# Optimization experiments

Measured on AMD Instinct MI355X. Metric: run time of the kernel, lower is better.

The kernel has to match this reference:

```python
import jax, jax.numpy as jnp
import numpy as np

T, N, H = 256, 64, 512
DT, GAMMA, EPS = 0.01, 1.0, 1.0

def setup_inputs() -> dict:
    key = jax.random.key(0)
    ks = jax.random.split(key, 6)
    s = 1.0 / np.sqrt(H)  # keep recurrent dynamics stable
    return {
        "x": jax.random.normal(ks[0], (T, N, H), jnp.float32),
        "connection_matrix": (jax.random.uniform(ks[1], (N, N)) < 0.5).astype(jnp.float32),
        "W_h": jax.random.normal(ks[2], (N, H, H), jnp.float32) * s,
        "W_x": jax.random.normal(ks[3], (N, H, H), jnp.float32) * s,
        "b": jax.random.normal(ks[4], (N, H), jnp.float32) * 0.1,
        "initial_states": jnp.zeros((N, 2, H), jnp.float32),
    }

def reference(x, connection_matrix, W_h, W_x, b, initial_states):
    # x: (T, N, H); states: (N, 2, H) with states[:,0] = h_y (the archetype output)
    def step(carry, x_t):
        states, outs = carry
        # message passing: mix previous outputs through the connection matrix,
        # then gate with the external input (elementwise)
        new_ins = (connection_matrix @ outs) * x_t                      # (N, H)
        hy, hz = states[:, 0], states[:, 1]
        # batched RON cell over all N archetypes
        pre = (jnp.einsum('nij,nj->ni', W_h, hy)
               + jnp.einsum('nij,nj->ni', W_x, new_ins) + b)            # (N, H)
        hz_n = hz + DT * (jnp.tanh(pre) - GAMMA * hy - EPS * hz)
        hy_n = hy + DT * hz_n
        new_states = jnp.stack([hy_n, hz_n], axis=1)                    # (N, 2, H)
        return (new_states, hy_n), (new_states, new_ins)

    init_outs = jnp.zeros_like(x[0])  # initial_outs=None path in the original
    _, (states_seq, ins_seq) = jax.lax.scan(step, (initial_states, init_outs), x)
    # original prepends the initial state and x[0] to the returned lists
    states_all = jnp.concatenate([initial_states[None], states_seq], axis=0)  # (T+1, N, 2, H)
    ins_all = jnp.concatenate([x[:1], ins_seq], axis=0)                       # (T+1, N, H)
    return states_all, ins_all
```

## Files before the change

### kernel.cpp

```cpp
#include <hip/hip_runtime.h>

constexpr int   T_ = 256, N_ = 64, H_ = 512;
constexpr float DT_ = 0.01f, GAMMA_ = 1.0f, EPS_ = 1.0f;

constexpr int GRID  = 256;
constexpr int BLOCK = 1024;
constexpr int WGPN  = GRID / N_;
constexpr int ROWS  = H_ / WGPN;
constexpr int WAVES = BLOCK / 64;
constexpr int RPW   = ROWS / WAVES;
constexpr int LJ    = 4;

__device__ __forceinline__ void grid_barrier(unsigned* cnt, unsigned* gen,
                                             unsigned target) {
    __syncthreads();
    if (threadIdx.x == 0) {
        __threadfence();
        unsigned prev = __hip_atomic_fetch_add(cnt, 1u, __ATOMIC_ACQ_REL,
                                               __HIP_MEMORY_SCOPE_AGENT);
        if (prev == (unsigned)GRID - 1u) {
            __hip_atomic_store(cnt, 0u, __ATOMIC_RELAXED,
                               __HIP_MEMORY_SCOPE_AGENT);
            __hip_atomic_fetch_add(gen, 1u, __ATOMIC_RELEASE,
                                   __HIP_MEMORY_SCOPE_AGENT);
        } else {
            while (__hip_atomic_load(gen, __ATOMIC_ACQUIRE,
                                     __HIP_MEMORY_SCOPE_AGENT) < target)
                __builtin_amdgcn_s_sleep(1);
        }
    }
    __syncthreads();
    __threadfence();
}

__global__ __launch_bounds__(BLOCK, 4)
void archetypes_persistent(const float* __restrict__ x,
                           const float* __restrict__ conn,
                           const float* __restrict__ W_h,
                           const float* __restrict__ W_x,
                           const float* __restrict__ bias,
                           const float* __restrict__ init_states,
                           float* __restrict__ out,
                           unsigned* __restrict__ bar)
{
    const int tid  = threadIdx.x;
    const int wg   = blockIdx.x;
    const int n    = wg / WGPN;
    const int q    = wg % WGPN;
    const int lane = tid & 63;
    const int wave = tid >> 6;

    float* states_all = out;
    float* ins_all    = out + (size_t)(T_ + 1) * N_ * 2 * H_;

    __shared__ float s_wx[LJ * WAVES][H_];
    __shared__ float s_hy[H_];
    __shared__ float s_ins[H_];
    __shared__ float s_pre[ROWS];
    __shared__ float s_conn[N_];
    __shared__ float s_bias[ROWS];

    const float4* Wh4 = (const float4*)(W_h + ((size_t)n * H_ + q * ROWS) * H_);
    const float4* Wx4 = (const float4*)(W_x + ((size_t)n * H_ + q * ROWS) * H_);

    float4 wh_reg[RPW][2];
    float4 wx_reg[RPW - LJ][2];
    #pragma unroll
    for (int j = 0; j < RPW; ++j) {
        const int r_l = wave + WAVES * j;
        wh_reg[j][0] = Wh4[r_l * (H_ / 4) + lane];
        wh_reg[j][1] = Wh4[r_l * (H_ / 4) + 64 + lane];
    }
    #pragma unroll
    for (int j = LJ; j < RPW; ++j) {
        const int r_l = wave + WAVES * j;
        wx_reg[j - LJ][0] = Wx4[r_l * (H_ / 4) + lane];
        wx_reg[j - LJ][1] = Wx4[r_l * (H_ / 4) + 64 + lane];
    }
    {
        float4* dst = (float4*)&s_wx[0][0];
        for (int idx = tid; idx < LJ * WAVES * (H_ / 4); idx += BLOCK)
            dst[idx] = Wx4[idx];
    }
    if (tid < N_)   s_conn[tid] = conn[n * N_ + tid];
    if (tid < ROWS) s_bias[tid] = bias[n * H_ + q * ROWS + tid];

    for (int idx = wg * BLOCK + tid; idx < N_ * 2 * H_; idx += GRID * BLOCK)
        states_all[idx] = init_states[idx];
    for (int idx = wg * BLOCK + tid; idx < N_ * H_; idx += GRID * BLOCK)
        ins_all[idx] = x[idx];

    unsigned* cnt = bar;
    unsigned* gen = bar + 1;
    unsigned bt = 0;

    grid_barrier(cnt, gen, ++bt);

    const int half = tid >> 9;
    const int h    = tid & (H_ - 1);

    for (int t = 0; t < T_; ++t) {
        const float* st_t = states_all + (size_t)t * N_ * 2 * H_;

        if (!half) {
            float i0 = 0.f;
            if (t > 0) {
                float a = 0.f;
                #pragma unroll 8
                for (int m = 0; m < N_; ++m)
                    a += s_conn[m] * st_t[m * 2 * H_ + h];
                i0 = a * x[(size_t)t * N_ * H_ + n * H_ + h];
            }
            s_ins[h] = i0;
            float* insd = ins_all + (size_t)(t + 1) * N_ * H_ + n * H_;
            if (h / ROWS == q) insd[h] = i0;
        } else {
            s_hy[h] = st_t[n * 2 * H_ + h];
        }
        __syncthreads();

        {
            const float4* vh = (const float4*)s_hy;
            const float4* vi = (const float4*)s_ins;
            const float4 v0 = vh[lane], v1 = vh[64 + lane];
            const float4 u0 = vi[lane], u1 = vi[64 + lane];
            #pragma unroll
            for (int j = 0; j < RPW; ++j) {
                const int r_l = wave + WAVES * j;
                float4 wx0, wx1;
                if (j < LJ) {
                    const float4* lx = (const float4*)&s_wx[r_l][0];
                    wx0 = lx[lane];
                    wx1 = lx[64 + lane];
                } else {
                    wx0 = wx_reg[j - LJ][0];
                    wx1 = wx_reg[j - LJ][1];
                }
                float acc = 0.f;
                acc += wh_reg[j][0].x * v0.x + wh_reg[j][0].y * v0.y +
                       wh_reg[j][0].z * v0.z + wh_reg[j][0].w * v0.w;
                acc += wx0.x * u0.x + wx0.y * u0.y + wx0.z * u0.z + wx0.w * u0.w;
                acc += wh_reg[j][1].x * v1.x + wh_reg[j][1].y * v1.y +
                       wh_reg[j][1].z * v1.z + wh_reg[j][1].w * v1.w;
                acc += wx1.x * u1.x + wx1.y * u1.y + wx1.z * u1.z + wx1.w * u1.w;
                #pragma unroll
                for (int off = 32; off; off >>= 1)
                    acc += __shfl_xor(acc, off);
                if (lane == 0) s_pre[r_l] = acc;
            }
        }
        __syncthreads();

        if (tid < ROWS) {
            const int i    = q * ROWS + tid;
            const float pre  = s_pre[tid] + s_bias[tid];
            const float hy   = s_hy[i];
            const float hz   = st_t[n * 2 * H_ + H_ + i];
            const float th   = tanhf(pre);
            const float hz_n = hz + DT_ * (th - GAMMA_ * hy - EPS_ * hz);
            const float hy_n = hy + DT_ * hz_n;
            float* st1 = states_all + (size_t)(t + 1) * N_ * 2 * H_ + n * 2 * H_;
            st1[i]      = hy_n;
            st1[H_ + i] = hz_n;
        }

        grid_barrier(cnt, gen, ++bt);
    }
}

constexpr int FGRID = 1024, FBLOCK = 256, FWGPN = 16, FROWS = 32, FRPW = 8;

__global__ __launch_bounds__(FBLOCK)
void archetypes_init(const float* __restrict__ x,
                     const float* __restrict__ init_states,
                     float* __restrict__ out)
{
    float* states_all = out;
    float* ins_all    = out + (size_t)(T_ + 1) * N_ * 2 * H_;
    const int idx = blockIdx.x * FBLOCK + threadIdx.x;
    if (idx < N_ * 2 * H_) states_all[idx] = init_states[idx];
    if (idx < N_ * H_)     ins_all[idx]    = x[idx];
}

__global__ __launch_bounds__(FBLOCK)
void archetypes_step(int t,
                     const float* __restrict__ x,
                     const float* __restrict__ conn,
                     const float* __restrict__ W_h,
                     const float* __restrict__ W_x,
                     const float* __restrict__ bias,
                     float* __restrict__ out)
{
    const int tid  = threadIdx.x;
    const int wg   = blockIdx.x;
    const int n    = wg / FWGPN;
    const int q    = wg % FWGPN;
    const int lane = tid & 63;
    const int wave = tid >> 6;

    float* states_all = out;
    float* ins_all    = out + (size_t)(T_ + 1) * N_ * 2 * H_;

    __shared__ float s_hy[H_];
    __shared__ float s_ins[H_];
    __shared__ float s_pre[FROWS];
    __shared__ float s_conn[N_];
    __shared__ float s_bias[FROWS];

    if (tid < N_)    s_conn[tid] = conn[n * N_ + tid];
    if (tid < FROWS) s_bias[tid] = bias[n * H_ + q * FROWS + tid];
    __syncthreads();

    const float* st_t = states_all + (size_t)t * N_ * 2 * H_;
    {
        const int h0 = tid, h1 = tid + 256;
        float i0 = 0.f, i1 = 0.f;
        if (t > 0) {
            const float* xr = x + (size_t)t * N_ * H_ + n * H_;
            float a0 = 0.f, a1 = 0.f;
            #pragma unroll 8
            for (int m = 0; m < N_; ++m) {
                const float c = s_conn[m];
                a0 += c * st_t[m * 2 * H_ + h0];
                a1 += c * st_t[m * 2 * H_ + h1];
            }
            i0 = a0 * xr[h0];
            i1 = a1 * xr[h1];
        }
        s_ins[h0] = i0;
        s_ins[h1] = i1;
        s_hy[h0] = st_t[n * 2 * H_ + h0];
        s_hy[h1] = st_t[n * 2 * H_ + h1];
        float* insd = ins_all + (size_t)(t + 1) * N_ * H_ + n * H_;
        if (h0 / FROWS == q) insd[h0] = i0;
        if (h1 / FROWS == q) insd[h1] = i1;
    }
    __syncthreads();
    {
        const float4* vh = (const float4*)s_hy;
        const float4* vi = (const float4*)s_ins;
        const float4* Wh4 = (const float4*)(W_h + ((size_t)n * H_ + q * FROWS) * H_);
        const float4* Wx4 = (const float4*)(W_x + ((size_t)n * H_ + q * FROWS) * H_);
        const float4 v0 = vh[lane], v1 = vh[64 + lane];
        const float4 u0 = vi[lane], u1 = vi[64 + lane];
        #pragma unroll
        for (int j = 0; j < FRPW; ++j) {
            const int r_l = wave + 4 * j;
            const float4 a0 = Wh4[r_l * (H_ / 4) + lane];
            const float4 a1 = Wh4[r_l * (H_ / 4) + 64 + lane];
            const float4 wx0 = Wx4[r_l * (H_ / 4) + lane];
            const float4 wx1 = Wx4[r_l * (H_ / 4) + 64 + lane];
            float acc = 0.f;
            acc += a0.x * v0.x + a0.y * v0.y + a0.z * v0.z + a0.w * v0.w;
            acc += wx0.x * u0.x + wx0.y * u0.y + wx0.z * u0.z + wx0.w * u0.w;
            acc += a1.x * v1.x + a1.y * v1.y + a1.z * v1.z + a1.w * v1.w;
            acc += wx1.x * u1.x + wx1.y * u1.y + wx1.z * u1.z + wx1.w * u1.w;
            #pragma unroll
            for (int off = 32; off; off >>= 1)
                acc += __shfl_xor(acc, off);
            if (lane == 0) s_pre[r_l] = acc;
        }
    }
    __syncthreads();
    if (tid < FROWS) {
        const int i   = q * FROWS + tid;
        const float pre  = s_pre[tid] + s_bias[tid];
        const float hy   = st_t[n * 2 * H_ + i];
        const float hz   = st_t[n * 2 * H_ + H_ + i];
        const float th   = tanhf(pre);
        const float hz_n = hz + DT_ * (th - GAMMA_ * hy - EPS_ * hz);
        const float hy_n = hy + DT_ * hz_n;
        float* st1 = states_all + (size_t)(t + 1) * N_ * 2 * H_ + n * 2 * H_;
        st1[i]      = hy_n;
        st1[H_ + i] = hz_n;
    }
}

extern "C" void kernel_launch(void* const* d_in, const int* in_sizes, int n_in,
                              void* d_out, int out_size, void* d_ws, size_t ws_size,
                              hipStream_t stream) {
    const float* x     = (const float*)d_in[0];
    const float* conn  = (const float*)d_in[1];
    const float* W_h   = (const float*)d_in[2];
    const float* W_x   = (const float*)d_in[3];
    const float* bias  = (const float*)d_in[4];
    const float* inits = (const float*)d_in[5];
    float*       outp  = (float*)d_out;
    unsigned*    bar   = (unsigned*)d_ws;

    int perCU = 0;
    (void)hipOccupancyMaxActiveBlocksPerMultiprocessor(
        &perCU, (const void*)archetypes_persistent, BLOCK, 0);
    const bool coop_ok = (perCU * 256 >= GRID);

    if (coop_ok) {
        hipMemsetAsync(bar, 0, 2 * sizeof(unsigned), stream);
        void* args[] = {(void*)&x, (void*)&conn, (void*)&W_h, (void*)&W_x,
                        (void*)&bias, (void*)&inits, (void*)&outp, (void*)&bar};
        hipLaunchCooperativeKernel((void*)archetypes_persistent,
                                   dim3(GRID), dim3(BLOCK), args, 0, stream);
    } else {
        archetypes_init<<<dim3((N_ * 2 * H_ + FBLOCK - 1) / FBLOCK), dim3(FBLOCK),
                          0, stream>>>(x, inits, outp);
        for (int t = 0; t < T_; ++t)
            archetypes_step<<<dim3(FGRID), dim3(FBLOCK), 0, stream>>>(
                t, x, conn, W_h, W_x, bias, outp);
    }
}
```

Measured before the change: 6.730 ms.

## Replace generation-counter grid barrier with per-step hierarchical arrival flags

Swaps the single shared counter/generation grid barrier for per-timestep flags. Each archetype's workgroups increment a per-network counter, and the last arrival bumps a padded per-step ready counter that every block polls before reading that step's states. This spreads atomic contention across many addresses and drops the second barrier sync, in exchange for a larger workspace that must be zeroed by a memset on every launch. It still needs all 64 networks before each step, so the dependency structure is unchanged and the saving is mainly in barrier latency.

```diff
diff --git a/kernel.cpp b/kernel.cpp
--- a/kernel.cpp
+++ b/kernel.cpp
@@ -10,27 +10,10 @@
 constexpr int WAVES = BLOCK / 64;
 constexpr int RPW   = ROWS / WAVES;
 constexpr int LJ    = 4;
-
-__device__ __forceinline__ void grid_barrier(unsigned* cnt, unsigned* gen,
-                                             unsigned target) {
-    __syncthreads();
-    if (threadIdx.x == 0) {
-        __threadfence();
-        unsigned prev = __hip_atomic_fetch_add(cnt, 1u, __ATOMIC_ACQ_REL,
-                                               __HIP_MEMORY_SCOPE_AGENT);
-        if (prev == (unsigned)GRID - 1u) {
-            __hip_atomic_store(cnt, 0u, __ATOMIC_RELAXED,
-                               __HIP_MEMORY_SCOPE_AGENT);
-            __hip_atomic_fetch_add(gen, 1u, __ATOMIC_RELEASE,
-                                   __HIP_MEMORY_SCOPE_AGENT);
-        } else {
-            while (__hip_atomic_load(gen, __ATOMIC_ACQUIRE,
-                                     __HIP_MEMORY_SCOPE_AGENT) < target)
-                __builtin_amdgcn_s_sleep(1);
-        }
-    }
-    __syncthreads();
-    __threadfence();
+constexpr int SR_STRIDE = 16;
+
+__device__ __forceinline__ unsigned ld_relaxed(const unsigned* p) {
+    return __hip_atomic_load(p, __ATOMIC_RELAXED, __HIP_MEMORY_SCOPE_AGENT);
 }
 
 __global__ __launch_bounds__(BLOCK, 4)
@@ -41,7 +24,8 @@
                            const float* __restrict__ bias,
                            const float* __restrict__ init_states,
                            float* __restrict__ out,
-                           unsigned* __restrict__ bar)
+                           unsigned* __restrict__ step_ready,
+                           unsigned* __restrict__ net_arrive)
 {
     const int tid  = threadIdx.x;
     const int wg   = blockIdx.x;
@@ -85,21 +69,29 @@
     if (tid < N_)   s_conn[tid] = conn[n * N_ + tid];
     if (tid < ROWS) s_bias[tid] = bias[n * H_ + q * ROWS + tid];
 
-    for (int idx = wg * BLOCK + tid; idx < N_ * 2 * H_; idx += GRID * BLOCK)
-        states_all[idx] = init_states[idx];
-    for (int idx = wg * BLOCK + tid; idx < N_ * H_; idx += GRID * BLOCK)
-        ins_all[idx] = x[idx];
-
-    unsigned* cnt = bar;
-    unsigned* gen = bar + 1;
-    unsigned bt = 0;
-
-    grid_barrier(cnt, gen, ++bt);
+    states_all[n * 2 * H_ + tid] = init_states[n * 2 * H_ + tid];
+    if (tid < H_) ins_all[n * H_ + tid] = x[n * H_ + tid];
+    __syncthreads();
+    if (tid == 0) {
+        __threadfence();
+        unsigned prev = __hip_atomic_fetch_add(&net_arrive[n], 1u,
+                            __ATOMIC_ACQ_REL, __HIP_MEMORY_SCOPE_AGENT);
+        if (prev == WGPN - 1)
+            __hip_atomic_fetch_add(&step_ready[0], 1u,
+                            __ATOMIC_RELEASE, __HIP_MEMORY_SCOPE_AGENT);
+    }
 
     const int half = tid >> 9;
     const int h    = tid & (H_ - 1);
 
     for (int t = 0; t < T_; ++t) {
+        if (tid == 0) {
+            while (ld_relaxed(&step_ready[t * SR_STRIDE]) < (unsigned)N_)
+                __builtin_amdgcn_s_sleep(1);
+            __threadfence();
+        }
+        __syncthreads();
+
         const float* st_t = states_all + (size_t)t * N_ * 2 * H_;
 
         if (!half) {
@@ -163,8 +155,15 @@
             st1[i]      = hy_n;
             st1[H_ + i] = hz_n;
         }
-
-        grid_barrier(cnt, gen, ++bt);
+        __syncthreads();
+        if (tid == 0) {
+            __threadfence();
+            unsigned prev = __hip_atomic_fetch_add(&net_arrive[(t + 1) * N_ + n],
+                                1u, __ATOMIC_ACQ_REL, __HIP_MEMORY_SCOPE_AGENT);
+            if (prev == WGPN - 1)
+                __hip_atomic_fetch_add(&step_ready[(t + 1) * SR_STRIDE], 1u,
+                                __ATOMIC_RELEASE, __HIP_MEMORY_SCOPE_AGENT);
+        }
     }
 }
 
@@ -286,17 +285,22 @@
     const float* bias  = (const float*)d_in[4];
     const float* inits = (const float*)d_in[5];
     float*       outp  = (float*)d_out;
-    unsigned*    bar   = (unsigned*)d_ws;
+
+    unsigned* step_ready = (unsigned*)d_ws;
+    unsigned* net_arrive = step_ready + (size_t)(T_ + 1) * SR_STRIDE;
+    const size_t flag_bytes =
+        sizeof(unsigned) * ((size_t)(T_ + 1) * SR_STRIDE + (size_t)(T_ + 1) * N_);
 
     int perCU = 0;
     (void)hipOccupancyMaxActiveBlocksPerMultiprocessor(
         &perCU, (const void*)archetypes_persistent, BLOCK, 0);
-    const bool coop_ok = (perCU * 256 >= GRID);
+    const bool coop_ok = (perCU * 256 >= GRID) && (ws_size >= flag_bytes);
 
     if (coop_ok) {
-        hipMemsetAsync(bar, 0, 2 * sizeof(unsigned), stream);
+        hipMemsetAsync(d_ws, 0, flag_bytes, stream);
         void* args[] = {(void*)&x, (void*)&conn, (void*)&W_h, (void*)&W_x,
-                        (void*)&bias, (void*)&inits, (void*)&outp, (void*)&bar};
+                        (void*)&bias, (void*)&inits, (void*)&outp,
+                        (void*)&step_ready, (void*)&net_arrive};
         hipLaunchCooperativeKernel((void*)archetypes_persistent,
                                    dim3(GRID), dim3(BLOCK), args, 0, stream);
     } else {
```

Measured after the change: 6.820 ms. No clear change (+1.3%).
